# Performance work log

Measured on AMD Instinct MI355X. Metric: run time of the kernel, lower is better.

## Reference

```python
import jax, jax.numpy as jnp
import numpy as np

H = 128; W = 128          # BEV grid (row_num_embed = col_num_embed = 128)
B = 1
CIN = 384; D = 256; NH = 8; NP = 4; NF = 128  # NF = num_feats of pos encoding
NLAYERS = 4               # 3 cross + 1 self


def setup_inputs() -> dict:
    key = jax.random.key(0)
    ks = jax.random.split(key, 32)
    s = 0.02
    rn = lambda k, shp: (jax.random.normal(k, shp, dtype=jnp.float32) * s)
    z = lambda shp: jnp.zeros(shp, jnp.float32)
    inp = {
        'query': jax.random.normal(ks[0], (B, CIN, H, W), jnp.float32),
        'value': jax.random.normal(ks[1], (B, CIN, H, W), jnp.float32),
        # 1x1 conv input projections (out, in)
        'conv_q_w': rn(ks[2], (D, CIN)), 'conv_q_b': z((D,)),
        'conv_v_w': rn(ks[3], (D, CIN)), 'conv_v_b': z((D,)),
        # learned positional embedding tables
        'row_embed': rn(ks[4], (H, NF)), 'col_embed': rn(ks[5], (W, NF)),
        # pre-attention linear layers (in, out)
        'lin_q_w': rn(ks[6], (D, D)), 'lin_q_b': z((D,)),
        'lin_v_w': rn(ks[7], (D, D)), 'lin_v_b': z((D,)),
        # stacked MSDeformAttn params for 4 layers
        'msda_off_w': rn(ks[8], (NLAYERS, D, NH * NP * 2)), 'msda_off_b': z((NLAYERS, NH * NP * 2)),
        'msda_aw_w': rn(ks[9], (NLAYERS, D, NH * NP)), 'msda_aw_b': z((NLAYERS, NH * NP)),
        'msda_vp_w': rn(ks[10], (NLAYERS, D, D)), 'msda_vp_b': z((NLAYERS, D)),
        'msda_op_w': rn(ks[11], (NLAYERS, D, D)), 'msda_op_b': z((NLAYERS, D)),
        # output MLP: 256 -> 128 -> 64 -> 384 with LayerNorm+ReLU between
        'out_w1': rn(ks[12], (D, D // 2)), 'out_b1': z((D // 2,)),
        'ln1_g': jnp.ones((D // 2,), jnp.float32), 'ln1_b': z((D // 2,)),
        'out_w2': rn(ks[13], (D // 2, D // 4)), 'out_b2': z((D // 4,)),
        'ln2_g': jnp.ones((D // 4,), jnp.float32), 'ln2_b': z((D // 4,)),
        'out_w3': rn(ks[14], (D // 4, CIN)), 'out_b3': z((CIN,)),
    }
    return inp


def _ln(x, g, b):
    mu = jnp.mean(x, -1, keepdims=True)
    var = jnp.mean(jnp.square(x - mu), -1, keepdims=True)
    return (x - mu) * jax.lax.rsqrt(var + 1e-5) * g + b


def reference(query, value, conv_q_w, conv_q_b, conv_v_w, conv_v_b, row_embed, col_embed,
              lin_q_w, lin_q_b, lin_v_w, lin_v_b,
              msda_off_w, msda_off_b, msda_aw_w, msda_aw_b,
              msda_vp_w, msda_vp_b, msda_op_w, msda_op_b,
              out_w1, out_b1, ln1_g, ln1_b, out_w2, out_b2, ln2_g, ln2_b, out_w3, out_b3):
    Bv, Cin, Hh, Ww = query.shape
    Nq = Hh * Ww
    HD = D // NH
    # 1x1 convs = per-pixel channel matmul; layout (Nq, B, D) = flatten(2).permute(2,0,1)
    q = jnp.einsum('bchw,dc->hwbd', query, conv_q_w).reshape(Nq, Bv, D) + conv_q_b
    v = jnp.einsum('bchw,dc->hwbd', value, conv_v_w).reshape(Nq, Bv, D) + conv_v_b
    # LearnedPositionalEncoding: cat([col_embed(x), row_embed(y)], -1)
    pos = jnp.concatenate([
        jnp.broadcast_to(col_embed[None, :Ww], (Hh, Ww, NF)),
        jnp.broadcast_to(row_embed[:Hh, None], (Hh, Ww, NF))], -1).reshape(Nq, 1, D)
    q = q @ lin_q_w + lin_q_b
    v = v @ lin_v_w + lin_v_b
    # reference points (pixel centers, normalized, (x, y) order)
    ry = (jnp.arange(Hh, dtype=q.dtype) + 0.5) / Hh
    rx = (jnp.arange(Ww, dtype=q.dtype) + 0.5) / Ww
    gx, gy = jnp.meshgrid(rx, ry, indexing='xy')  # (H, W)
    ref = jnp.stack([gx, gy], -1).reshape(1, Nq, 2)
    inv_wh = jnp.array([1.0 / Ww, 1.0 / Hh], dtype=q.dtype)

    def msda_layer(q_in, v_in, i):
        qp = q_in + pos                                   # query + query_pos
        val = (v_in @ msda_vp_w[i] + msda_vp_b[i]).transpose(1, 0, 2).reshape(Bv, Hh, Ww, NH, HD)
        off = (qp @ msda_off_w[i] + msda_off_b[i]).transpose(1, 0, 2).reshape(Bv, Nq, NH, NP, 2)
        aw = jax.nn.softmax((qp @ msda_aw_w[i] + msda_aw_b[i]).transpose(1, 0, 2)
                            .reshape(Bv, Nq, NH, NP), axis=-1)
        loc = ref[:, :, None, None, :] + off * inv_wh     # (B, Nq, NH, NP, 2) in [0,1]
        # bilinear sampling, zero padding, align_corners=False (grid_sample semantics)
        x = loc[..., 0] * Ww - 0.5
        y = loc[..., 1] * Hh - 0.5
        x0f = jnp.floor(x); y0f = jnp.floor(y)
        lx = (x - x0f).transpose(0, 2, 1, 3)              # (B, NH, Nq, NP)
        ly = (y - y0f).transpose(0, 2, 1, 3)
        x0 = x0f.astype(jnp.int32).transpose(0, 2, 1, 3)
        y0 = y0f.astype(jnp.int32).transpose(0, 2, 1, 3)
        vflat = val.transpose(0, 3, 1, 2, 4).reshape(Bv, NH, Hh * Ww, HD)
        awt = aw.transpose(0, 2, 1, 3)                    # (B, NH, Nq, NP)

        def corner(yi, xi, w):
            valid = (yi >= 0) & (yi < Hh) & (xi >= 0) & (xi < Ww)
            idx = (jnp.clip(yi, 0, Hh - 1) * Ww + jnp.clip(xi, 0, Ww - 1)).reshape(Bv, NH, Nq * NP, 1)
            g = jnp.take_along_axis(vflat, idx, axis=2).reshape(Bv, NH, Nq, NP, HD)
            return g * (w * valid.astype(w.dtype) * awt)[..., None]

        out = (corner(y0, x0, (1 - lx) * (1 - ly))
               + corner(y0, x0 + 1, lx * (1 - ly))
               + corner(y0 + 1, x0, (1 - lx) * ly)
               + corner(y0 + 1, x0 + 1, lx * ly)).sum(3)  # (B, NH, Nq, HD)
        out = out.transpose(2, 0, 1, 3).reshape(Nq, Bv, D)
        return out @ msda_op_w[i] + msda_op_b[i] + q_in   # residual (dropout=identity, eval)

    for i in range(3):                                    # cross layers: value features
        q = msda_layer(q, v, i)
    q = msda_layer(q, q, 3)                               # self layer: value = query

    h1 = jax.nn.relu(_ln(q @ out_w1 + out_b1, ln1_g, ln1_b))
    h2 = jax.nn.relu(_ln(h1 @ out_w2 + out_b2, ln2_g, ln2_b))
    out = h2 @ out_w3 + out_b3                            # (Nq, B, Cin)
    return out.transpose(1, 2, 0).reshape(Bv, Cin, Hh, Ww)
```

## Files before the change

kernel.cpp:

```cpp
#include <hip/hip_runtime.h>
#include <hip/hip_bf16.h>

#define NQ   16384
#define DIM  256

using bf16 = __hip_bfloat16;
using bf16x8 = __attribute__((ext_vector_type(8))) short;
using f32x4  = __attribute__((ext_vector_type(4))) float;

__device__ __forceinline__ float b2f(bf16 x) { return __bfloat162float(x); }
__device__ __forceinline__ bf16  f2b(float x) { return __float2bfloat16(x); }
__device__ __forceinline__ unsigned short f2bb(float x) {
    bf16 h = __float2bfloat16(x);
    return *(unsigned short*)&h;
}
__device__ __forceinline__ float us2f(unsigned short u) {
    unsigned int x = ((unsigned int)u) << 16;
    return __builtin_bit_cast(float, x);
}

__device__ __forceinline__ void xcd_map(int& sx, int& sy)
{
    const int gx  = gridDim.x;
    const int nwg = gridDim.x * gridDim.y;
    const int bid = blockIdx.y * gx + blockIdx.x;
    const int q = nwg >> 3, r = nwg & 7;
    const int xcd = bid & 7, sl = bid >> 3;
    const int s = (xcd < r ? xcd * (q + 1) : r * (q + 1) + (xcd - r) * q) + sl;
    sx = s % gx;
    sy = s / gx;
}

template<int MW, int NF, int KS>
__device__ __forceinline__ void gcore(
    bf16* __restrict__ Bs,
    const bf16* __restrict__ A, const bf16* __restrict__ Bgl,
    const float* __restrict__ bias, const bf16* __restrict__ res,
    const bf16* __restrict__ pos, bf16* __restrict__ C, bf16* __restrict__ C2,
    int N, int n0, int m0)
{
    constexpr int K   = KS * 32;
    constexpr int LDB = K + 8;

    const int t    = threadIdx.x;
    const int lane = t & 63;
    const int wid  = t >> 6;
    const int lr   = lane & 15;
    const int lg   = lane >> 4;

    const bf16* Ab = A + (size_t)(m0 + wid * MW * 16 + lr) * K + lg * 8;

    bf16x8 af0[MW], af1[MW], af2[MW];
#pragma unroll
    for (int mi = 0; mi < MW; ++mi)
        af0[mi] = *(const bf16x8*)&Ab[(size_t)(mi * 16) * K + 0];
    if (KS > 1) {
#pragma unroll
        for (int mi = 0; mi < MW; ++mi)
            af1[mi] = *(const bf16x8*)&Ab[(size_t)(mi * 16) * K + 32];
    }

#pragma unroll
    for (int c = 0; c < NF * KS / 4; ++c) {
        const int id  = c * 256 + t;
        const int row = id / (KS * 4);
        const int kc  = id % (KS * 4);
        *(int4*)&Bs[row * LDB + kc * 8] = *(const int4*)&Bgl[(size_t)row * K + kc * 8];
    }
    __syncthreads();

    f32x4 acc[MW][NF];
#pragma unroll
    for (int i = 0; i < MW; ++i)
#pragma unroll
        for (int j = 0; j < NF; ++j) {
            f32x4 z = {0.f, 0.f, 0.f, 0.f};
            acc[i][j] = z;
        }

    bf16x8 bcur[NF], bnxt[NF];
#pragma unroll
    for (int jj = 0; jj < NF; ++jj)
        bcur[jj] = *(const bf16x8*)&Bs[(jj * 16 + lr) * LDB + lg * 8];

#pragma unroll
    for (int s = 0; s < KS; ++s) {
        if (s + 2 < KS) {
#pragma unroll
            for (int mi = 0; mi < MW; ++mi)
                af2[mi] = *(const bf16x8*)&Ab[(size_t)(mi * 16) * K + (s + 2) * 32];
        }
        if (s + 1 < KS) {
#pragma unroll
            for (int jj = 0; jj < NF; ++jj)
                bnxt[jj] = *(const bf16x8*)&Bs[(jj * 16 + lr) * LDB + (s + 1) * 32 + lg * 8];
        }
#pragma unroll
        for (int mi = 0; mi < MW; ++mi)
#pragma unroll
            for (int jj = 0; jj < NF; ++jj)
                acc[mi][jj] = __builtin_amdgcn_mfma_f32_16x16x32_bf16(
                    af0[mi], bcur[jj], acc[mi][jj], 0, 0, 0);
#pragma unroll
        for (int mi = 0; mi < MW; ++mi) { af0[mi] = af1[mi]; af1[mi] = af2[mi]; }
#pragma unroll
        for (int jj = 0; jj < NF; ++jj) bcur[jj] = bnxt[jj];
    }

    const bool dores = res != nullptr;
    const bool doqp  = C2 != nullptr;
#pragma unroll
    for (int mi = 0; mi < MW; ++mi) {
#pragma unroll
        for (int jj = 0; jj < NF; ++jj) {
            const int row0 = m0 + wid * MW * 16 + mi * 16 + lg * 4;
            const int col  = n0 + jj * 16 + lr;
            const float bvl = bias[col];
#pragma unroll
            for (int r = 0; r < 4; ++r) {
                const size_t off = (size_t)(row0 + r) * N + col;
                float v = acc[mi][jj][r] + bvl;
                if (dores) v += b2f(res[off]);
                C[off] = f2b(v);
                if (doqp) {
                    const size_t poff = (size_t)(row0 + r) * 256 + col;
                    C2[poff] = f2b(v + b2f(pos[poff]));
                }
            }
        }
    }
}

template<int MW, int KS>
__global__ __launch_bounds__(256)
void gmm_std(const bf16* __restrict__ A, const bf16* __restrict__ B,
             const float* __restrict__ bias, const bf16* __restrict__ res,
             const bf16* __restrict__ pos, bf16* __restrict__ C, bf16* __restrict__ C2,
             int N)
{
    __shared__ bf16 Bs[64 * (KS * 32 + 8)];
    int sx, sy;
    xcd_map(sx, sy);
    const int n0 = sx * 64;
    gcore<MW, 4, KS>(Bs, A, B + (size_t)n0 * (KS * 32), bias, res, pos, C, C2,
                     N, n0, sy * (MW * 64));
}

__global__ __launch_bounds__(256)
void gmm_qv(const bf16* __restrict__ QT, const bf16* __restrict__ WQ,
            const float* __restrict__ BQ, bf16* __restrict__ QA, bf16* __restrict__ QPb,
            const bf16* __restrict__ VT, const bf16* __restrict__ WV,
            const float* __restrict__ BV, bf16* __restrict__ V,
            const bf16* __restrict__ pos)
{
    __shared__ bf16 Bs[64 * (384 + 8)];
    int sx, sy;
    xcd_map(sx, sy);
    const int m0 = sy * 128;
    if (sx < 4) {
        const int n0 = sx * 64;
        gcore<2, 4, 12>(Bs, QT, WQ + (size_t)n0 * 384, BQ, nullptr, pos,
                        QA, QPb, 256, n0, m0);
    } else {
        const int n0 = (sx - 4) * 64;
        gcore<2, 4, 12>(Bs, VT, WV + (size_t)n0 * 384, BV, nullptr, nullptr,
                        V, nullptr, 256, n0, m0);
    }
}

__global__ __launch_bounds__(256)
void gmm_vpall(const bf16* __restrict__ V, const bf16* __restrict__ WVP,
               const float* __restrict__ vp_b, bf16* __restrict__ VP,
               const bf16* __restrict__ QPb, const bf16* __restrict__ Boa,
               const float* __restrict__ boa, bf16* __restrict__ OA)
{
    __shared__ bf16 Bs[64 * (256 + 8)];
    int sx, sy;
    xcd_map(sx, sy);
    const int m0 = sy * 64;
    if (sx < 12) {
        const int layer = sx >> 2;
        const int nloc  = (sx & 3) * 64;
        gcore<1, 4, 8>(Bs, V, WVP + (size_t)sx * 64 * 256,
                       vp_b + layer * 256, nullptr, nullptr,
                       VP + (size_t)layer * NQ * 256, nullptr, 256, nloc, m0);
    } else {
        const int n0 = (sx - 12) * 64;
        gcore<1, 4, 8>(Bs, QPb, Boa + (size_t)n0 * 256, boa, nullptr, nullptr,
                       OA, nullptr, 128, n0, m0);
    }
}

__global__ __launch_bounds__(256)
void gmm_vo3(const bf16* __restrict__ cur, const bf16* __restrict__ Bvp,
             const float* __restrict__ bvp, bf16* __restrict__ T2,
             const bf16* __restrict__ QPb, const bf16* __restrict__ Boa,
             const float* __restrict__ boa, bf16* __restrict__ OA)
{
    __shared__ bf16 Bs[64 * (256 + 8)];
    int sx, sy;
    xcd_map(sx, sy);
    const int m0 = sy * 64;
    if (sx < 4) {
        const int n0 = sx * 64;
        gcore<1, 4, 8>(Bs, cur, Bvp + (size_t)n0 * 256, bvp, nullptr, nullptr,
                       T2, nullptr, 256, n0, m0);
    } else {
        const int n0 = (sx - 4) * 64;
        gcore<1, 4, 8>(Bs, QPb, Boa + (size_t)n0 * 256, boa, nullptr, nullptr,
                       OA, nullptr, 128, n0, m0);
    }
}

template<int NF, int KS>
__device__ __forceinline__ void gcore_ln(
    bf16* __restrict__ Bs,
    const bf16* __restrict__ A, const bf16* __restrict__ Bgl,
    const float* __restrict__ bias, bf16* __restrict__ C,
    const float* __restrict__ lng, const float* __restrict__ lnb,
    int N, int m0)
{
    constexpr int K    = KS * 32;
    constexpr int LDB  = K + 8;
    constexpr int NPAN = NF * 16;

    const int t    = threadIdx.x;
    const int lane = t & 63;
    const int wid  = t >> 6;
    const int lr   = lane & 15;
    const int lg   = lane >> 4;

#pragma unroll
    for (int c = 0; c < NF * KS / 4; ++c) {
        const int id  = c * 256 + t;
        const int row = id / (KS * 4);
        const int kc  = id % (KS * 4);
        *(int4*)&Bs[row * LDB + kc * 8] = *(const int4*)&Bgl[(size_t)row * K + kc * 8];
    }
    __syncthreads();

    f32x4 acc[NF];
#pragma unroll
    for (int j = 0; j < NF; ++j) { f32x4 z = {0.f, 0.f, 0.f, 0.f}; acc[j] = z; }

    const bf16* Ab = A + (size_t)(m0 + wid * 16 + lr) * K + lg * 8;

#pragma unroll
    for (int s = 0; s < KS; ++s) {
        bf16x8 af = *(const bf16x8*)&Ab[s * 32];
#pragma unroll
        for (int jj = 0; jj < NF; ++jj) {
            const bf16x8 bf = *(const bf16x8*)&Bs[(jj * 16 + lr) * LDB + s * 32 + lg * 8];
            acc[jj] = __builtin_amdgcn_mfma_f32_16x16x32_bf16(af, bf, acc[jj], 0, 0, 0);
        }
    }

    float bvl[NF], gv[NF], bb[NF];
#pragma unroll
    for (int jj = 0; jj < NF; ++jj) {
        const int col = jj * 16 + lr;
        bvl[jj] = bias[col]; gv[jj] = lng[col]; bb[jj] = lnb[col];
    }
#pragma unroll
    for (int r = 0; r < 4; ++r) {
        float v[NF];
        float s = 0.f;
#pragma unroll
        for (int jj = 0; jj < NF; ++jj) { v[jj] = acc[jj][r] + bvl[jj]; s += v[jj]; }
        s += __shfl_xor(s, 1); s += __shfl_xor(s, 2);
        s += __shfl_xor(s, 4); s += __shfl_xor(s, 8);
        const float mu = s * (1.f / NPAN);
        float vs = 0.f;
#pragma unroll
        for (int jj = 0; jj < NF; ++jj) { const float d = v[jj] - mu; vs += d * d; }
        vs += __shfl_xor(vs, 1); vs += __shfl_xor(vs, 2);
        vs += __shfl_xor(vs, 4); vs += __shfl_xor(vs, 8);
        const float rstd = rsqrtf(vs * (1.f / NPAN) + 1e-5f);
        const int row = m0 + wid * 16 + lg * 4 + r;
#pragma unroll
        for (int jj = 0; jj < NF; ++jj) {
            const float o = (v[jj] - mu) * rstd * gv[jj] + bb[jj];
            C[(size_t)row * N + jj * 16 + lr] = f2b(fmaxf(o, 0.f));
        }
    }
}

__global__ __launch_bounds__(256)
void gmm_mlp1(const bf16* __restrict__ A, const bf16* __restrict__ B,
              const float* __restrict__ bias, bf16* __restrict__ C,
              const float* __restrict__ g, const float* __restrict__ b)
{
    __shared__ bf16 Bs[128 * (256 + 8)];
    gcore_ln<8, 8>(Bs, A, B, bias, C, g, b, 128, blockIdx.y * 64);
}

__global__ __launch_bounds__(256)
void gmm_mlp2(const bf16* __restrict__ A, const bf16* __restrict__ B,
              const float* __restrict__ bias, bf16* __restrict__ C,
              const float* __restrict__ g, const float* __restrict__ b)
{
    __shared__ bf16 Bs[64 * (128 + 8)];
    gcore_ln<4, 4>(Bs, A, B, bias, C, g, b, 64, blockIdx.y * 64);
}

__global__ __launch_bounds__(256)
void transpose_in(const float* __restrict__ q, const float* __restrict__ v,
                  bf16* __restrict__ QT, bf16* __restrict__ VT)
{
    __shared__ float tile[64][68];
    const float* in = blockIdx.z ? v : q;
    bf16* out = blockIdx.z ? VT : QT;
    const int t = threadIdx.x;
    const int c0 = blockIdx.x * 64, m0 = blockIdx.y * 64;
    const int tr = t >> 4;
    const int tc4 = (t & 15) * 4;
#pragma unroll
    for (int i = 0; i < 4; ++i) {
        const int c = i * 16 + tr;
        const float4 vv = *(const float4*)&in[(size_t)(c0 + c) * NQ + m0 + tc4];
        tile[tc4 + 0][c] = vv.x; tile[tc4 + 1][c] = vv.y;
        tile[tc4 + 2][c] = vv.z; tile[tc4 + 3][c] = vv.w;
    }
    __syncthreads();
#pragma unroll
    for (int i = 0; i < 4; ++i) {
        const int m = i * 16 + tr;
        ushort4 o;
        o.x = f2bb(tile[m][tc4 + 0]); o.y = f2bb(tile[m][tc4 + 1]);
        o.z = f2bb(tile[m][tc4 + 2]); o.w = f2bb(tile[m][tc4 + 3]);
        *(ushort4*)&out[(size_t)(m0 + m) * 384 + c0 + tc4] = o;
    }
}

__global__ __launch_bounds__(256)
void transpose_out(const bf16* __restrict__ in, float* __restrict__ out)
{
    __shared__ float tile[64][68];
    const int t = threadIdx.x;
    const int c0 = blockIdx.x * 64, m0 = blockIdx.y * 64;
    const int tr = t >> 4;
    const int tc4 = (t & 15) * 4;
#pragma unroll
    for (int i = 0; i < 4; ++i) {
        const int m = i * 16 + tr;
        const ushort4 v = *(const ushort4*)&in[(size_t)(m0 + m) * 384 + c0 + tc4];
        tile[tc4 + 0][m] = us2f(v.x);
        tile[tc4 + 1][m] = us2f(v.y);
        tile[tc4 + 2][m] = us2f(v.z);
        tile[tc4 + 3][m] = us2f(v.w);
    }
    __syncthreads();
#pragma unroll
    for (int i = 0; i < 4; ++i) {
        const int c = i * 16 + tr;
        float4 o;
        o.x = tile[c][tc4 + 0]; o.y = tile[c][tc4 + 1];
        o.z = tile[c][tc4 + 2]; o.w = tile[c][tc4 + 3];
        *(float4*)&out[(size_t)(c0 + c) * NQ + m0 + tc4] = o;
    }
}

__global__ __launch_bounds__(256)
void prep_weights(const float* __restrict__ vp_w, const float* __restrict__ op_w,
                  const float* __restrict__ off_w, const float* __restrict__ aw_w,
                  const float* __restrict__ off_b, const float* __restrict__ aw_b,
                  const float* __restrict__ w1, const float* __restrict__ w2,
                  const float* __restrict__ w3,
                  bf16* __restrict__ WVP, bf16* __restrict__ WOP, bf16* __restrict__ WOA,
                  bf16* __restrict__ WM1, bf16* __restrict__ WM2, bf16* __restrict__ WM3,
                  float* __restrict__ OAB)
{
    int idx = blockIdx.x * 256 + threadIdx.x;
    auto tr = [](const float* src, bf16* dst, int K, int N, int i) {
        const int n = i / K, k = i % K;
        dst[i] = __float2bfloat16(src[k * N + n]);
    };
    if (idx < 262144) { const int l = idx >> 16, r = idx & 65535; tr(vp_w + l * 65536, WVP + l * 65536, 256, 256, r); return; }
    idx -= 262144;
    if (idx < 262144) { const int l = idx >> 16, r = idx & 65535; tr(op_w + l * 65536, WOP + l * 65536, 256, 256, r); return; }
    idx -= 262144;
    if (idx < 65536) { const int l = idx >> 14, r = idx & 16383; tr(off_w + l * 16384, WOA + l * 32768, 256, 64, r); return; }
    idx -= 65536;
    if (idx < 32768) { const int l = idx >> 13, r = idx & 8191; tr(aw_w + l * 8192, WOA + l * 32768 + 16384, 256, 32, r); return; }
    idx -= 32768;
    if (idx < 32768) { const int l = idx >> 13, r = idx & 8191; WOA[l * 32768 + 24576 + r] = f2b(0.f); return; }
    idx -= 32768;
    if (idx < 32768) { tr(w1, WM1, 256, 128, idx); return; }
    idx -= 32768;
    if (idx < 8192) { tr(w2, WM2, 128, 64, idx); return; }
    idx -= 8192;
    if (idx < 24576) { tr(w3, WM3, 64, 384, idx); return; }
    idx -= 24576;
    if (idx < 512) {
        const int l = idx >> 7, r = idx & 127;
        OAB[idx] = (r < 64) ? off_b[l * 64 + r] : (r < 96 ? aw_b[l * 32 + r - 64] : 0.f);
    }
}

__global__ __launch_bounds__(256)
void prep_combined(const float* __restrict__ cqw, const float* __restrict__ cqb,
                   const float* __restrict__ cvw, const float* __restrict__ cvb,
                   const float* __restrict__ lqw, const float* __restrict__ lqb,
                   const float* __restrict__ lvw, const float* __restrict__ lvb,
                   bf16* __restrict__ WQ, bf16* __restrict__ WV,
                   float* __restrict__ BQ, float* __restrict__ BV)
{
    const int b = blockIdx.x;
    if (b < 768) {
        const bool isq = b < 384;
        const float* cw = isq ? cqw : cvw;
        const float* lw = isq ? lqw : lvw;
        bf16* W = isq ? WQ : WV;
        const int idx = (b % 384) * 256 + threadIdx.x;
        const int n = idx / 384, c = idx % 384;
        float s = 0.f;
        for (int d = 0; d < 256; ++d)
            s = fmaf(cw[d * 384 + c], lw[d * 256 + n], s);
        W[idx] = f2b(s);
    } else {
        const int n = threadIdx.x;
        float sq = lqb[n], sv = lvb[n];
        for (int d = 0; d < 256; ++d) {
            sq = fmaf(cqb[d], lqw[d * 256 + n], sq);
            sv = fmaf(cvb[d], lvw[d * 256 + n], sv);
        }
        BQ[n] = sq; BV[n] = sv;
    }
}

__global__ __launch_bounds__(256)
void pos_kernel(const float* __restrict__ row_embed, const float* __restrict__ col_embed,
                bf16* __restrict__ pos)
{
    const int idx = blockIdx.x * 256 + threadIdx.x;
    const int pix = idx >> 5, d0 = (idx & 31) * 8;
    const int h = pix >> 7, w = pix & 127;
    const float* src = (d0 < 128) ? &col_embed[w * 128 + d0] : &row_embed[h * 128 + (d0 - 128)];
    const float4 a = *(const float4*)src;
    const float4 b = *(const float4*)(src + 4);
    bf16x8 o;
    o[0] = (short)f2bb(a.x); o[1] = (short)f2bb(a.y);
    o[2] = (short)f2bb(a.z); o[3] = (short)f2bb(a.w);
    o[4] = (short)f2bb(b.x); o[5] = (short)f2bb(b.y);
    o[6] = (short)f2bb(b.z); o[7] = (short)f2bb(b.w);
    *(bf16x8*)&pos[(size_t)pix * 256 + d0] = o;
}

__global__ __launch_bounds__(256)
void sample_kernel(const bf16* __restrict__ val, const bf16* __restrict__ oa,
                   bf16* __restrict__ out)
{
    const int tid = threadIdx.x;
    const int pix = blockIdx.x * 8 + (tid >> 5);
    const int thr = tid & 31;
    const int head = thr >> 2;
    const int c0 = thr * 8;
    const float fx = (float)(pix & 127);
    const float fy = (float)(pix >> 7);
    const unsigned short* oap = (const unsigned short*)(oa + (size_t)pix * 128);
    const bf16x8 offs = *(const bf16x8*)&oap[head * 8];
    const ushort4 lg4 = *(const ushort4*)&oap[64 + head * 4];
    const float l0 = us2f(lg4.x), l1 = us2f(lg4.y), l2 = us2f(lg4.z), l3 = us2f(lg4.w);
    const float mx = fmaxf(fmaxf(l0, l1), fmaxf(l2, l3));
    const float e0 = __expf(l0 - mx), e1 = __expf(l1 - mx);
    const float e2 = __expf(l2 - mx), e3 = __expf(l3 - mx);
    const float inv = 1.f / (e0 + e1 + e2 + e3);
    const float aw4[4] = {e0 * inv, e1 * inv, e2 * inv, e3 * inv};

    float acc[8];
#pragma unroll
    for (int c = 0; c < 8; ++c) acc[c] = 0.f;

#pragma unroll
    for (int p = 0; p < 4; ++p) {
        const float x = fx + us2f((unsigned short)offs[p * 2 + 0]);
        const float y = fy + us2f((unsigned short)offs[p * 2 + 1]);
        const float x0f = floorf(x), y0f = floorf(y);
        const float lx = x - x0f, ly = y - y0f;
        const int x0 = (int)x0f, y0 = (int)y0f;
        const float a = aw4[p];
        const float wc[4] = {(1.f - lx) * (1.f - ly) * a, lx * (1.f - ly) * a,
                             (1.f - lx) * ly * a,         lx * ly * a};
        const int xs[4] = {x0, x0 + 1, x0, x0 + 1};
        const int ys[4] = {y0, y0, y0 + 1, y0 + 1};
#pragma unroll
        for (int k = 0; k < 4; ++k) {
            if ((unsigned)ys[k] < 128u && (unsigned)xs[k] < 128u) {
                const bf16x8 v = *(const bf16x8*)&val[(size_t)((ys[k] << 7) + xs[k]) * 256 + c0];
                const float w = wc[k];
#pragma unroll
                for (int c = 0; c < 8; ++c)
                    acc[c] = fmaf(us2f((unsigned short)v[c]), w, acc[c]);
            }
        }
    }
    bf16x8 o;
#pragma unroll
    for (int c = 0; c < 8; ++c) o[c] = (short)f2bb(acc[c]);
    *(bf16x8*)&out[(size_t)pix * 256 + c0] = o;
}

extern "C" void kernel_launch(void* const* d_in, const int* in_sizes, int n_in,
                              void* d_out, int out_size, void* d_ws, size_t ws_size,
                              hipStream_t stream)
{
    const float* query     = (const float*)d_in[0];
    const float* value     = (const float*)d_in[1];
    const float* conv_q_w  = (const float*)d_in[2];
    const float* conv_q_b  = (const float*)d_in[3];
    const float* conv_v_w  = (const float*)d_in[4];
    const float* conv_v_b  = (const float*)d_in[5];
    const float* row_embed = (const float*)d_in[6];
    const float* col_embed = (const float*)d_in[7];
    const float* lin_q_w   = (const float*)d_in[8];
    const float* lin_q_b   = (const float*)d_in[9];
    const float* lin_v_w   = (const float*)d_in[10];
    const float* lin_v_b   = (const float*)d_in[11];
    const float* off_w     = (const float*)d_in[12];
    const float* off_b     = (const float*)d_in[13];
    const float* aw_w      = (const float*)d_in[14];
    const float* aw_b      = (const float*)d_in[15];
    const float* vp_w      = (const float*)d_in[16];
    const float* vp_b      = (const float*)d_in[17];
    const float* op_w      = (const float*)d_in[18];
    const float* op_b      = (const float*)d_in[19];
    const float* out_w1    = (const float*)d_in[20];
    const float* out_b1    = (const float*)d_in[21];
    const float* ln1_g     = (const float*)d_in[22];
    const float* ln1_b     = (const float*)d_in[23];
    const float* out_w2    = (const float*)d_in[24];
    const float* out_b2    = (const float*)d_in[25];
    const float* ln2_g     = (const float*)d_in[26];
    const float* ln2_b     = (const float*)d_in[27];
    const float* out_w3    = (const float*)d_in[28];
    const float* out_b3    = (const float*)d_in[29];

    bf16* w = (bf16*)d_ws;
    auto alloc = [&](size_t n) { bf16* p = w; w += n; return p; };
    bf16* QT  = alloc((size_t)NQ * 384);
    bf16* VT  = alloc((size_t)NQ * 384);
    bf16* POS = alloc((size_t)NQ * 256);
    bf16* QA  = alloc((size_t)NQ * 256);
    bf16* QB  = alloc((size_t)NQ * 256);
    bf16* QPb = alloc((size_t)NQ * 256);
    bf16* V   = alloc((size_t)NQ * 256);
    bf16* T1  = alloc((size_t)NQ * 256);
    bf16* T2  = alloc((size_t)NQ * 256);
    bf16* VP  = alloc((size_t)3 * NQ * 256);
    bf16* OA  = alloc((size_t)NQ * 128);
    bf16* WQc = alloc(256 * 384);
    bf16* WVc = alloc(256 * 384);
    bf16* WVP = alloc(4 * 256 * 256);
    bf16* WOP = alloc(4 * 256 * 256);
    bf16* WOA = alloc(4 * 128 * 256);
    bf16* WM1 = alloc(128 * 256);
    bf16* WM2 = alloc(64 * 128);
    bf16* WM3 = alloc(384 * 64);
    float* fp = (float*)w;
    float* BQc = fp; fp += 256;
    float* BVc = fp; fp += 256;
    float* OAB = fp; fp += 512;

    const dim3 blk(256);

    transpose_in<<<dim3(6, 256, 2), blk, 0, stream>>>(query, value, QT, VT);
    prep_weights<<<2818, blk, 0, stream>>>(vp_w, op_w, off_w, aw_w, off_b, aw_b,
                                           out_w1, out_w2, out_w3,
                                           WVP, WOP, WOA, WM1, WM2, WM3, OAB);
    prep_combined<<<769, blk, 0, stream>>>(conv_q_w, conv_q_b, conv_v_w, conv_v_b,
                                           lin_q_w, lin_q_b, lin_v_w, lin_v_b,
                                           WQc, WVc, BQc, BVc);
    pos_kernel<<<2048, blk, 0, stream>>>(row_embed, col_embed, POS);

    gmm_qv<<<dim3(8, 128), blk, 0, stream>>>(
        QT, WQc, BQc, QA, QPb, VT, WVc, BVc, V, POS);
    gmm_vpall<<<dim3(14, 256), blk, 0, stream>>>(
        V, WVP, vp_b, VP, QPb, WOA, OAB, OA);

    bf16* cur = QA;
    bf16* nxt = QB;
    for (int i = 0; i < 4; ++i) {
        const bf16* valbuf;
        if (i < 3) {
            valbuf = VP + (size_t)i * NQ * 256;
            if (i > 0)
                gmm_std<1, 8><<<dim3(2, 256), blk, 0, stream>>>(
                    QPb, WOA + (size_t)i * 32768, OAB + i * 128, nullptr, nullptr,
                    OA, nullptr, 128);
        } else {
            valbuf = T2;
            gmm_vo3<<<dim3(6, 256), blk, 0, stream>>>(
                cur, WVP + (size_t)3 * 65536, vp_b + 3 * 256, T2,
                QPb, WOA + (size_t)3 * 32768, OAB + 3 * 128, OA);
        }
        sample_kernel<<<2048, blk, 0, stream>>>(valbuf, OA, T1);
        gmm_std<1, 8><<<dim3(4, 256), blk, 0, stream>>>(
            T1, WOP + (size_t)i * 65536, op_b + i * 256, cur, POS, nxt, QPb, 256);
        bf16* tmp = cur; cur = nxt; nxt = tmp;
    }

    gmm_mlp1<<<dim3(1, 256), blk, 0, stream>>>(cur, WM1, out_b1, T1, ln1_g, ln1_b);
    gmm_mlp2<<<dim3(1, 256), blk, 0, stream>>>(T1, WM2, out_b2, T2, ln2_g, ln2_b);
    gmm_std<1, 2><<<dim3(6, 256), blk, 0, stream>>>(
        T2, WM3, out_b3, nullptr, nullptr, QT, nullptr, 384);
    transpose_out<<<dim3(6, 256), blk, 0, stream>>>(QT, (float*)d_out);
}
```

Before: 246.2 us.

## Merge prep kernels into one launch and fuse final GEMM with output transpose

The four setup kernels (input transpose, weight conversion, combined weight folding, positional embedding) are merged into one launch that dispatches on block index. The last 64->384 GEMM now writes fp32 straight into the channel-major output layout, so the bf16 intermediate and the separate transpose kernel are gone. This cuts launch overhead and one round trip through global memory. In exchange the output stores are strided float4 writes per column, and the merged kernel's branches have uneven per-block cost.

```diff
diff --git a/kernel.cpp b/kernel.cpp
--- a/kernel.cpp
+++ b/kernel.cpp
@@ -212,6 +212,65 @@
     }
 }
 
+__global__ __launch_bounds__(256)
+void gmm_out(const bf16* __restrict__ A, const bf16* __restrict__ B,
+             const float* __restrict__ bias, float* __restrict__ out)
+{
+    constexpr int KS = 2, K = 64, LDB = K + 8;
+    __shared__ bf16 Bs[64 * LDB];
+    int sx, sy;
+    xcd_map(sx, sy);
+    const int n0 = sx * 64;
+    const int m0 = sy * 64;
+
+    const int t    = threadIdx.x;
+    const int lane = t & 63;
+    const int wid  = t >> 6;
+    const int lr   = lane & 15;
+    const int lg   = lane >> 4;
+
+    const bf16* Ab = A + (size_t)(m0 + wid * 16 + lr) * K + lg * 8;
+    const bf16* Bb = B + (size_t)n0 * K;
+
+    bf16x8 af0 = *(const bf16x8*)&Ab[0];
+    bf16x8 af1 = *(const bf16x8*)&Ab[32];
+
+#pragma unroll
+    for (int c = 0; c < 2; ++c) {
+        const int id  = c * 256 + t;
+        const int row = id >> 3, kc = id & 7;
+        *(int4*)&Bs[row * LDB + kc * 8] = *(const int4*)&Bb[(size_t)row * K + kc * 8];
+    }
+    __syncthreads();
+
+    f32x4 acc[4];
+#pragma unroll
+    for (int j = 0; j < 4; ++j) { f32x4 z = {0.f, 0.f, 0.f, 0.f}; acc[j] = z; }
+
+#pragma unroll
+    for (int s = 0; s < KS; ++s) {
+        const bf16x8 af = s == 0 ? af0 : af1;
+#pragma unroll
+        for (int jj = 0; jj < 4; ++jj) {
+            const bf16x8 bf = *(const bf16x8*)&Bs[(jj * 16 + lr) * LDB + s * 32 + lg * 8];
+            acc[jj] = __builtin_amdgcn_mfma_f32_16x16x32_bf16(af, bf, acc[jj], 0, 0, 0);
+        }
+    }
+
+    const int row0 = m0 + wid * 16 + lg * 4;
+#pragma unroll
+    for (int jj = 0; jj < 4; ++jj) {
+        const int col = n0 + jj * 16 + lr;
+        const float bvl = bias[col];
+        float4 o;
+        o.x = acc[jj][0] + bvl;
+        o.y = acc[jj][1] + bvl;
+        o.z = acc[jj][2] + bvl;
+        o.w = acc[jj][3] + bvl;
+        *(float4*)&out[(size_t)col * NQ + row0] = o;
+    }
+}
+
 template<int NF, int KS>
 __device__ __forceinline__ void gcore_ln(
     bf16* __restrict__ Bs,
@@ -304,146 +363,121 @@
 }
 
 __global__ __launch_bounds__(256)
-void transpose_in(const float* __restrict__ q, const float* __restrict__ v,
-                  bf16* __restrict__ QT, bf16* __restrict__ VT)
+void prep_all(const float* __restrict__ query, const float* __restrict__ value,
+              bf16* __restrict__ QT, bf16* __restrict__ VT,
+              const float* __restrict__ vp_w, const float* __restrict__ op_w,
+              const float* __restrict__ off_w, const float* __restrict__ aw_w,
+              const float* __restrict__ off_b, const float* __restrict__ aw_b,
+              const float* __restrict__ w1, const float* __restrict__ w2,
+              const float* __restrict__ w3,
+              bf16* __restrict__ WVP, bf16* __restrict__ WOP, bf16* __restrict__ WOA,
+              bf16* __restrict__ WM1, bf16* __restrict__ WM2, bf16* __restrict__ WM3,
+              float* __restrict__ OAB,
+              const float* __restrict__ cqw, const float* __restrict__ cqb,
+              const float* __restrict__ cvw, const float* __restrict__ cvb,
+              const float* __restrict__ lqw, const float* __restrict__ lqb,
+              const float* __restrict__ lvw, const float* __restrict__ lvb,
+              bf16* __restrict__ WQc, bf16* __restrict__ WVc,
+              float* __restrict__ BQc, float* __restrict__ BVc,
+              const float* __restrict__ row_embed, const float* __restrict__ col_embed,
+              bf16* __restrict__ POS)
 {
     __shared__ float tile[64][68];
-    const float* in = blockIdx.z ? v : q;
-    bf16* out = blockIdx.z ? VT : QT;
+    const int b = blockIdx.x;
     const int t = threadIdx.x;
-    const int c0 = blockIdx.x * 64, m0 = blockIdx.y * 64;
-    const int tr = t >> 4;
-    const int tc4 = (t & 15) * 4;
-#pragma unroll
-    for (int i = 0; i < 4; ++i) {
-        const int c = i * 16 + tr;
-        const float4 vv = *(const float4*)&in[(size_t)(c0 + c) * NQ + m0 + tc4];
-        tile[tc4 + 0][c] = vv.x; tile[tc4 + 1][c] = vv.y;
-        tile[tc4 + 2][c] = vv.z; tile[tc4 + 3][c] = vv.w;
-    }
-    __syncthreads();
-#pragma unroll
-    for (int i = 0; i < 4; ++i) {
-        const int m = i * 16 + tr;
-        ushort4 o;
-        o.x = f2bb(tile[m][tc4 + 0]); o.y = f2bb(tile[m][tc4 + 1]);
-        o.z = f2bb(tile[m][tc4 + 2]); o.w = f2bb(tile[m][tc4 + 3]);
-        *(ushort4*)&out[(size_t)(m0 + m) * 384 + c0 + tc4] = o;
-    }
-}
-
-__global__ __launch_bounds__(256)
-void transpose_out(const bf16* __restrict__ in, float* __restrict__ out)
-{
-    __shared__ float tile[64][68];
-    const int t = threadIdx.x;
-    const int c0 = blockIdx.x * 64, m0 = blockIdx.y * 64;
-    const int tr = t >> 4;
-    const int tc4 = (t & 15) * 4;
-#pragma unroll
-    for (int i = 0; i < 4; ++i) {
-        const int m = i * 16 + tr;
-        const ushort4 v = *(const ushort4*)&in[(size_t)(m0 + m) * 384 + c0 + tc4];
-        tile[tc4 + 0][m] = us2f(v.x);
-        tile[tc4 + 1][m] = us2f(v.y);
-        tile[tc4 + 2][m] = us2f(v.z);
-        tile[tc4 + 3][m] = us2f(v.w);
-    }
-    __syncthreads();
-#pragma unroll
-    for (int i = 0; i < 4; ++i) {
-        const int c = i * 16 + tr;
-        float4 o;
-        o.x = tile[c][tc4 + 0]; o.y = tile[c][tc4 + 1];
-        o.z = tile[c][tc4 + 2]; o.w = tile[c][tc4 + 3];
-        *(float4*)&out[(size_t)(c0 + c) * NQ + m0 + tc4] = o;
-    }
-}
-
-__global__ __launch_bounds__(256)
-void prep_weights(const float* __restrict__ vp_w, const float* __restrict__ op_w,
-                  const float* __restrict__ off_w, const float* __restrict__ aw_w,
-                  const float* __restrict__ off_b, const float* __restrict__ aw_b,
-                  const float* __restrict__ w1, const float* __restrict__ w2,
-                  const float* __restrict__ w3,
-                  bf16* __restrict__ WVP, bf16* __restrict__ WOP, bf16* __restrict__ WOA,
-                  bf16* __restrict__ WM1, bf16* __restrict__ WM2, bf16* __restrict__ WM3,
-                  float* __restrict__ OAB)
-{
-    int idx = blockIdx.x * 256 + threadIdx.x;
-    auto tr = [](const float* src, bf16* dst, int K, int N, int i) {
-        const int n = i / K, k = i % K;
-        dst[i] = __float2bfloat16(src[k * N + n]);
-    };
-    if (idx < 262144) { const int l = idx >> 16, r = idx & 65535; tr(vp_w + l * 65536, WVP + l * 65536, 256, 256, r); return; }
-    idx -= 262144;
-    if (idx < 262144) { const int l = idx >> 16, r = idx & 65535; tr(op_w + l * 65536, WOP + l * 65536, 256, 256, r); return; }
-    idx -= 262144;
-    if (idx < 65536) { const int l = idx >> 14, r = idx & 16383; tr(off_w + l * 16384, WOA + l * 32768, 256, 64, r); return; }
-    idx -= 65536;
-    if (idx < 32768) { const int l = idx >> 13, r = idx & 8191; tr(aw_w + l * 8192, WOA + l * 32768 + 16384, 256, 32, r); return; }
-    idx -= 32768;
-    if (idx < 32768) { const int l = idx >> 13, r = idx & 8191; WOA[l * 32768 + 24576 + r] = f2b(0.f); return; }
-    idx -= 32768;
-    if (idx < 32768) { tr(w1, WM1, 256, 128, idx); return; }
-    idx -= 32768;
-    if (idx < 8192) { tr(w2, WM2, 128, 64, idx); return; }
-    idx -= 8192;
-    if (idx < 24576) { tr(w3, WM3, 64, 384, idx); return; }
-    idx -= 24576;
-    if (idx < 512) {
-        const int l = idx >> 7, r = idx & 127;
-        OAB[idx] = (r < 64) ? off_b[l * 64 + r] : (r < 96 ? aw_b[l * 32 + r - 64] : 0.f);
-    }
-}
-
-__global__ __launch_bounds__(256)
-void prep_combined(const float* __restrict__ cqw, const float* __restrict__ cqb,
-                   const float* __restrict__ cvw, const float* __restrict__ cvb,
-                   const float* __restrict__ lqw, const float* __restrict__ lqb,
-                   const float* __restrict__ lvw, const float* __restrict__ lvb,
-                   bf16* __restrict__ WQ, bf16* __restrict__ WV,
-                   float* __restrict__ BQ, float* __restrict__ BV)
-{
-    const int b = blockIdx.x;
-    if (b < 768) {
-        const bool isq = b < 384;
-        const float* cw = isq ? cqw : cvw;
-        const float* lw = isq ? lqw : lvw;
-        bf16* W = isq ? WQ : WV;
-        const int idx = (b % 384) * 256 + threadIdx.x;
-        const int n = idx / 384, c = idx % 384;
-        float s = 0.f;
-        for (int d = 0; d < 256; ++d)
-            s = fmaf(cw[d * 384 + c], lw[d * 256 + n], s);
-        W[idx] = f2b(s);
-    } else {
-        const int n = threadIdx.x;
-        float sq = lqb[n], sv = lvb[n];
-        for (int d = 0; d < 256; ++d) {
-            sq = fmaf(cqb[d], lqw[d * 256 + n], sq);
-            sv = fmaf(cvb[d], lvw[d * 256 + n], sv);
-        }
-        BQ[n] = sq; BV[n] = sv;
-    }
-}
-
-__global__ __launch_bounds__(256)
-void pos_kernel(const float* __restrict__ row_embed, const float* __restrict__ col_embed,
-                bf16* __restrict__ pos)
-{
-    const int idx = blockIdx.x * 256 + threadIdx.x;
-    const int pix = idx >> 5, d0 = (idx & 31) * 8;
-    const int h = pix >> 7, w = pix & 127;
-    const float* src = (d0 < 128) ? &col_embed[w * 128 + d0] : &row_embed[h * 128 + (d0 - 128)];
-    const float4 a = *(const float4*)src;
-    const float4 b = *(const float4*)(src + 4);
-    bf16x8 o;
-    o[0] = (short)f2bb(a.x); o[1] = (short)f2bb(a.y);
-    o[2] = (short)f2bb(a.z); o[3] = (short)f2bb(a.w);
-    o[4] = (short)f2bb(b.x); o[5] = (short)f2bb(b.y);
-    o[6] = (short)f2bb(b.z); o[7] = (short)f2bb(b.w);
-    *(bf16x8*)&pos[(size_t)pix * 256 + d0] = o;
+
+    if (b < 3072) {
+        const int z = b / 1536, rem = b % 1536;
+        const float* in = z ? value : query;
+        bf16* out = z ? VT : QT;
+        const int c0 = (rem % 6) * 64, m0 = (rem / 6) * 64;
+        const int tr = t >> 4;
+        const int tc4 = (t & 15) * 4;
+#pragma unroll
+        for (int i = 0; i < 4; ++i) {
+            const int c = i * 16 + tr;
+            const float4 vv = *(const float4*)&in[(size_t)(c0 + c) * NQ + m0 + tc4];
+            tile[tc4 + 0][c] = vv.x; tile[tc4 + 1][c] = vv.y;
+            tile[tc4 + 2][c] = vv.z; tile[tc4 + 3][c] = vv.w;
+        }
+        __syncthreads();
+#pragma unroll
+        for (int i = 0; i < 4; ++i) {
+            const int m = i * 16 + tr;
+            ushort4 o;
+            o.x = f2bb(tile[m][tc4 + 0]); o.y = f2bb(tile[m][tc4 + 1]);
+            o.z = f2bb(tile[m][tc4 + 2]); o.w = f2bb(tile[m][tc4 + 3]);
+            *(ushort4*)&out[(size_t)(m0 + m) * 384 + c0 + tc4] = o;
+        }
+        return;
+    }
+    if (b < 5890) {
+        int idx = (b - 3072) * 256 + t;
+        auto tr = [](const float* src, bf16* dst, int K, int N, int i) {
+            const int n = i / K, k = i % K;
+            dst[i] = __float2bfloat16(src[k * N + n]);
+        };
+        if (idx < 262144) { const int l = idx >> 16, r = idx & 65535; tr(vp_w + l * 65536, WVP + l * 65536, 256, 256, r); return; }
+        idx -= 262144;
+        if (idx < 262144) { const int l = idx >> 16, r = idx & 65535; tr(op_w + l * 65536, WOP + l * 65536, 256, 256, r); return; }
+        idx -= 262144;
+        if (idx < 65536) { const int l = idx >> 14, r = idx & 16383; tr(off_w + l * 16384, WOA + l * 32768, 256, 64, r); return; }
+        idx -= 65536;
+        if (idx < 32768) { const int l = idx >> 13, r = idx & 8191; tr(aw_w + l * 8192, WOA + l * 32768 + 16384, 256, 32, r); return; }
+        idx -= 32768;
+        if (idx < 32768) { const int l = idx >> 13, r = idx & 8191; WOA[l * 32768 + 24576 + r] = f2b(0.f); return; }
+        idx -= 32768;
+        if (idx < 32768) { tr(w1, WM1, 256, 128, idx); return; }
+        idx -= 32768;
+        if (idx < 8192) { tr(w2, WM2, 128, 64, idx); return; }
+        idx -= 8192;
+        if (idx < 24576) { tr(w3, WM3, 64, 384, idx); return; }
+        idx -= 24576;
+        if (idx < 512) {
+            const int l = idx >> 7, r = idx & 127;
+            OAB[idx] = (r < 64) ? off_b[l * 64 + r] : (r < 96 ? aw_b[l * 32 + r - 64] : 0.f);
+        }
+        return;
+    }
+    if (b < 6659) {
+        const int bb = b - 5890;
+        if (bb < 768) {
+            const bool isq = bb < 384;
+            const float* cw = isq ? cqw : cvw;
+            const float* lw = isq ? lqw : lvw;
+            bf16* W = isq ? WQc : WVc;
+            const int idx = (bb % 384) * 256 + t;
+            const int n = idx / 384, c = idx % 384;
+            float s = 0.f;
+            for (int d = 0; d < 256; ++d)
+                s = fmaf(cw[d * 384 + c], lw[d * 256 + n], s);
+            W[idx] = f2b(s);
+        } else {
+            const int n = t;
+            float sq = lqb[n], sv = lvb[n];
+            for (int d = 0; d < 256; ++d) {
+                sq = fmaf(cqb[d], lqw[d * 256 + n], sq);
+                sv = fmaf(cvb[d], lvw[d * 256 + n], sv);
+            }
+            BQc[n] = sq; BVc[n] = sv;
+        }
+        return;
+    }
+    {
+        const int idx = (b - 6659) * 256 + t;
+        const int pix = idx >> 5, d0 = (idx & 31) * 8;
+        const int h = pix >> 7, w = pix & 127;
+        const float* src = (d0 < 128) ? &col_embed[w * 128 + d0]
+                                      : &row_embed[h * 128 + (d0 - 128)];
+        const float4 a = *(const float4*)src;
+        const float4 c = *(const float4*)(src + 4);
+        bf16x8 o;
+        o[0] = (short)f2bb(a.x); o[1] = (short)f2bb(a.y);
+        o[2] = (short)f2bb(a.z); o[3] = (short)f2bb(a.w);
+        o[4] = (short)f2bb(c.x); o[5] = (short)f2bb(c.y);
+        o[6] = (short)f2bb(c.z); o[7] = (short)f2bb(c.w);
+        *(bf16x8*)&POS[(size_t)pix * 256 + d0] = o;
+    }
 }
 
 __global__ __launch_bounds__(256)
@@ -563,14 +597,14 @@
 
     const dim3 blk(256);
 
-    transpose_in<<<dim3(6, 256, 2), blk, 0, stream>>>(query, value, QT, VT);
-    prep_weights<<<2818, blk, 0, stream>>>(vp_w, op_w, off_w, aw_w, off_b, aw_b,
-                                           out_w1, out_w2, out_w3,
-                                           WVP, WOP, WOA, WM1, WM2, WM3, OAB);
-    prep_combined<<<769, blk, 0, stream>>>(conv_q_w, conv_q_b, conv_v_w, conv_v_b,
-                                           lin_q_w, lin_q_b, lin_v_w, lin_v_b,
-                                           WQc, WVc, BQc, BVc);
-    pos_kernel<<<2048, blk, 0, stream>>>(row_embed, col_embed, POS);
+    prep_all<<<8707, blk, 0, stream>>>(
+        query, value, QT, VT,
+        vp_w, op_w, off_w, aw_w, off_b, aw_b, out_w1, out_w2, out_w3,
+        WVP, WOP, WOA, WM1, WM2, WM3, OAB,
+        conv_q_w, conv_q_b, conv_v_w, conv_v_b,
+        lin_q_w, lin_q_b, lin_v_w, lin_v_b,
+        WQc, WVc, BQc, BVc,
+        row_embed, col_embed, POS);
 
     gmm_qv<<<dim3(8, 128), blk, 0, stream>>>(
         QT, WQc, BQc, QA, QPb, VT, WVc, BVc, V, POS);
@@ -601,7 +635,5 @@
 
     gmm_mlp1<<<dim3(1, 256), blk, 0, stream>>>(cur, WM1, out_b1, T1, ln1_g, ln1_b);
     gmm_mlp2<<<dim3(1, 256), blk, 0, stream>>>(T1, WM2, out_b2, T2, ln2_g, ln2_b);
-    gmm_std<1, 2><<<dim3(6, 256), blk, 0, stream>>>(
-        T2, WM3, out_b3, nullptr, nullptr, QT, nullptr, 384);
-    transpose_out<<<dim3(6, 256), blk, 0, stream>>>(QT, (float*)d_out);
-}
+    gmm_out<<<dim3(6, 256), blk, 0, stream>>>(T2, WM3, out_b3, (float*)d_out);
+}
```

New measurement: 245.3 us. About the same (-0.3%).
